# Performance work log

Hardware: AMD Instinct MI355X
Metric: run time of the kernel (lower is better)

The kernel has to match this reference:

```python
import jax, jax.numpy as jnp
import numpy as np

N_NODES = 50000
N_EDGES = 600000
N_COMM = 500
COMM_EDGES = 8000
NFEAT = 128
NHID = 128
NCLASS = 10
NLAYERS = 3
NHEADS = 8
EPS = 1e-5


def setup_inputs() -> dict:
    key = jax.random.key(0)
    ks = jax.random.split(key, 32)
    s = 0.05
    def rn(i, shape, scale=s):
        return (jax.random.normal(ks[i], shape, dtype=jnp.float32) * scale)
    return {
        "node_features": jax.random.normal(ks[0], (N_NODES, NFEAT), dtype=jnp.float32),
        "node_edge_index": jax.random.randint(ks[1], (2, N_EDGES), 0, N_NODES),
        "comm_features": jax.random.normal(ks[2], (N_COMM, NHID), dtype=jnp.float32),
        "comm_edge_index": jax.random.randint(ks[3], (2, COMM_EDGES), 0, N_COMM),
        "node_to_comm_map": jax.random.randint(ks[4], (N_NODES,), 0, N_COMM),
        # node-branch GCN params (nfeat == nhid so weights stack)
        "node_W": rn(5, (NLAYERS, NHID, NHID)),
        "node_b": rn(6, (NLAYERS, NHID)),
        "node_bn_g": 1.0 + rn(7, (NLAYERS, NHID)),
        "node_bn_b": rn(8, (NLAYERS, NHID)),
        # community-branch GCN params
        "comm_W": rn(9, (NLAYERS, NHID, NHID)),
        "comm_b": rn(10, (NLAYERS, NHID)),
        "comm_bn_g": 1.0 + rn(11, (NLAYERS, NHID)),
        "comm_bn_b": rn(12, (NLAYERS, NHID)),
        # MultiheadAttention params (torch layout: y = x @ W.T + b)
        "attn_in_w": rn(13, (3 * NHID, NHID)),
        "attn_in_b": rn(14, (3 * NHID,)),
        "attn_out_w": rn(15, (NHID, NHID)),
        "attn_out_b": rn(16, (NHID,)),
        # gate LayerNorm
        "ln_g": 1.0 + rn(17, (NHID,)),
        "ln_b": rn(18, (NHID,)),
        # classifier: Linear(128,64) -> BN -> ReLU -> Linear(64,10)
        "cls_W1": rn(19, (NHID, NHID // 2)),
        "cls_b1": rn(20, (NHID // 2,)),
        "cls_bn_g": 1.0 + rn(21, (NHID // 2,)),
        "cls_bn_b": rn(22, (NHID // 2,)),
        "cls_W2": rn(23, (NHID // 2, NCLASS)),
        "cls_b2": rn(24, (NCLASS,)),
    }


def _gcn_norm(edge_index, n):
    # PyG gcn_norm: add self-loops, symmetric D^-1/2 (A+I) D^-1/2
    loop = jnp.arange(n)
    src = jnp.concatenate([edge_index[0], loop])
    dst = jnp.concatenate([edge_index[1], loop])
    deg = jax.ops.segment_sum(jnp.ones(src.shape[0], jnp.float32), dst, num_segments=n)
    dinv = jnp.where(deg > 0, deg ** -0.5, 0.0)
    return src, dst, dinv[src] * dinv[dst]


def _gcn_stack(x, edge_index, Ws, bs, gs, betas):
    n = x.shape[0]
    src, dst, norm = _gcn_norm(edge_index, n)
    h = x
    for i in range(Ws.shape[0]):
        h_prev = h
        m = h @ Ws[i]  # linear commutes with normalized aggregation
        agg = jax.ops.segment_sum(m[src] * norm[:, None], dst, num_segments=n) + bs[i]
        mu = agg.mean(0)
        var = agg.var(0)  # biased, as torch BN training
        hb = (agg - mu) / jnp.sqrt(var + EPS) * gs[i] + betas[i]
        h = jax.nn.relu(hb)
        if i > 0:
            h = h + h_prev
    return h


def _mha(x, wi, bi, wo, bo):
    # x: [N, S=2, E]
    N, S, E = x.shape
    dh = E // NHEADS
    qkv = x @ wi.T + bi
    q, k, v = jnp.split(qkv, 3, axis=-1)
    q = q.reshape(N, S, NHEADS, dh)
    k = k.reshape(N, S, NHEADS, dh)
    v = v.reshape(N, S, NHEADS, dh)
    att = jnp.einsum('nqhd,nkhd->nhqk', q, k) / np.float32(np.sqrt(dh))
    att = jax.nn.softmax(att, axis=-1)
    o = jnp.einsum('nhqk,nkhd->nqhd', att, v).reshape(N, S, E)
    return o @ wo.T + bo


def reference(node_features, node_edge_index, comm_features, comm_edge_index,
              node_to_comm_map, node_W, node_b, node_bn_g, node_bn_b,
              comm_W, comm_b, comm_bn_g, comm_bn_b,
              attn_in_w, attn_in_b, attn_out_w, attn_out_b,
              ln_g, ln_b, cls_W1, cls_b1, cls_bn_g, cls_bn_b, cls_W2, cls_b2):
    h_node = _gcn_stack(node_features, node_edge_index, node_W, node_b, node_bn_g, node_bn_b)
    h_comm = _gcn_stack(comm_features, comm_edge_index, comm_W, comm_b, comm_bn_g, comm_bn_b)
    safe = jnp.clip(node_to_comm_map, 0, h_comm.shape[0] - 1)
    h_comm_exp = h_comm[safe]  # [N, nhid] cross-scale gather
    comb = jnp.stack([h_node, h_comm_exp], axis=1)  # [N, 2, nhid]
    attended = _mha(comb, attn_in_w, attn_in_b, attn_out_w, attn_out_b)
    x = attended.mean(axis=1) + h_node
    mu = x.mean(-1, keepdims=True)
    var = x.var(-1, keepdims=True)
    h_final = (x - mu) / jnp.sqrt(var + EPS) * ln_g + ln_b
    z = h_final @ cls_W1 + cls_b1
    zm = z.mean(0)
    zv = z.var(0)
    z = jax.nn.relu((z - zm) / jnp.sqrt(zv + EPS) * cls_bn_g + cls_bn_b)
    logits = z @ cls_W2 + cls_b2
    return jax.nn.log_softmax(logits, axis=-1)
```

## Files before the change

kernel.cpp:

```cpp
#include <hip/hip_runtime.h>
#include <hip/hip_bf16.h>
#include <cstdint>
#include <cstddef>


typedef __attribute__((ext_vector_type(8))) short bf16x8;
typedef __attribute__((ext_vector_type(4))) float f32x4;

#define EPSV 1e-5f

__device__ __forceinline__ float b2f(unsigned short u) {
    union { unsigned int i; float f; } x; x.i = ((unsigned int)u) << 16; return x.f;
}
__device__ __forceinline__ unsigned short f2b(float f) {
    union { float f; unsigned int i; } x; x.f = f;
    unsigned int i = x.i;
    return (unsigned short)((i + 0x7fffu + ((i >> 16) & 1u)) >> 16);
}

__global__ void prep_kernel(const float* __restrict__ node_W, const float* __restrict__ comm_W,
                            const float* __restrict__ cls_W1, const float* __restrict__ attn_in_w,
                            const float* __restrict__ attn_out_w, const float* __restrict__ comm_feat,
                            const float* __restrict__ node_feat,
                            unsigned short* __restrict__ WtN, unsigned short* __restrict__ WtC,
                            unsigned short* __restrict__ W1t, unsigned short* __restrict__ WinB,
                            unsigned short* __restrict__ WoutB, unsigned short* __restrict__ cfb,
                            unsigned short* __restrict__ nfb, int nC128, int nN128) {
    int idx = blockIdx.x * 256 + threadIdx.x;
    if (idx < 49152) {
        int l = idx >> 14, e = idx & 16383;
        int j = e & 7, lane = (e >> 3) & 63, kc = (e >> 9) & 3, t = e >> 11;
        int col = t * 16 + (lane & 15);
        int k = (lane >> 4) * 8 + kc * 32 + j;
        WtN[idx] = f2b(node_W[l * 16384 + k * 128 + col]); return;
    }
    idx -= 49152;
    if (idx < 49152) {
        int l = idx >> 14, e = idx & 16383;
        int j = e & 7, lane = (e >> 3) & 63, kc = (e >> 9) & 3, t = e >> 11;
        int col = t * 16 + (lane & 15);
        int k = (lane >> 4) * 8 + kc * 32 + j;
        WtC[idx] = f2b(comm_W[l * 16384 + k * 128 + col]); return;
    }
    idx -= 49152;
    if (idx < 8192) {
        int e = idx;
        int j = e & 7, lane = (e >> 3) & 63, kc = (e >> 9) & 3, t = e >> 11;
        int col = t * 16 + (lane & 15);
        int k = (lane >> 4) * 8 + kc * 32 + j;
        W1t[idx] = f2b(cls_W1[k * 64 + col]); return;
    }
    idx -= 8192;
    if (idx < 49152) {
        int e = idx;
        int j = e & 7, lane = (e >> 3) & 63, kc = (e >> 9) & 3, t = e >> 11;
        int col = t * 16 + (lane & 15);
        int k = (lane >> 4) * 8 + kc * 32 + j;
        WinB[idx] = f2b(attn_in_w[col * 128 + k]); return;
    }
    idx -= 49152;
    if (idx < 16384) {
        int e = idx;
        int j = e & 7, lane = (e >> 3) & 63, kc = (e >> 9) & 3, t = e >> 11;
        int col = t * 16 + (lane & 15);
        int k = (lane >> 4) * 8 + kc * 32 + j;
        WoutB[idx] = f2b(attn_out_w[col * 128 + k]); return;
    }
    idx -= 16384;
    if (idx < nC128) { cfb[idx] = f2b(comm_feat[idx]); return; }
    idx -= nC128;
    if (idx < nN128) { nfb[idx] = f2b(node_feat[idx]); }
}

__global__ void count_dual(const int* __restrict__ nd, int* __restrict__ cnt_n, int nE,
                           const int* __restrict__ cd, int* __restrict__ cnt_c, int cE) {
    int t = blockIdx.x * 256 + threadIdx.x;
    if (t < nE) atomicAdd(&cnt_n[nd[t]], 1);
    else if (t - nE < cE) atomicAdd(&cnt_c[cd[t - nE]], 1);
}

__global__ void dinv_dual(const int* __restrict__ cnt_n, float* __restrict__ di_n, int nN,
                          const int* __restrict__ cnt_c, float* __restrict__ di_c, int nC) {
    int t = blockIdx.x * 256 + threadIdx.x;
    if (t < nN) di_n[t] = rsqrtf((float)cnt_n[t] + 1.0f);
    else if (t - nN < nC) di_c[t - nN] = rsqrtf((float)cnt_c[t - nN] + 1.0f);
}

__global__ void scan_block_dual(const int* __restrict__ cnt_n, int* __restrict__ rs_n,
                                int* __restrict__ bsum_n, int nN, int nbN,
                                const int* __restrict__ cnt_c, int* __restrict__ rs_c,
                                int* __restrict__ bsum_c, int nC) {
    __shared__ int tmp[2048];
    const int* cnt; int* excl; int* bsum; int n, lb;
    if ((int)blockIdx.x < nbN) { cnt = cnt_n; excl = rs_n; bsum = bsum_n; n = nN; lb = blockIdx.x; }
    else { cnt = cnt_c; excl = rs_c; bsum = bsum_c; n = nC; lb = blockIdx.x - nbN; }
    int tid = threadIdx.x;
    int gid = lb * 1024 + tid;
    int v = (gid < n) ? ((cnt[gid] + 7) & ~7) : 0;
    int buf = 0;
    tmp[tid] = v;
    __syncthreads();
    for (int d = 1; d < 1024; d <<= 1) {
        int t = tmp[buf * 1024 + tid];
        int add = (tid >= d) ? tmp[buf * 1024 + tid - d] : 0;
        tmp[(1 - buf) * 1024 + tid] = t + add;
        buf = 1 - buf;
        __syncthreads();
    }
    int inc = tmp[buf * 1024 + tid];
    if (gid < n) excl[gid] = inc - v;
    if (tid == 1023) bsum[lb] = inc;
}

__global__ void scan_sums_dual(int* __restrict__ bsum_n, int nbN,
                               int* __restrict__ bsum_c, int nbC) {
    if (threadIdx.x == 0) {
        int acc = 0;
        for (int i = 0; i < nbN; ++i) { int t = bsum_n[i]; bsum_n[i] = acc; acc += t; }
    } else if (threadIdx.x == 1) {
        int acc = 0;
        for (int i = 0; i < nbC; ++i) { int t = bsum_c[i]; bsum_c[i] = acc; acc += t; }
    }
}

__global__ void scan_add_dual(int* __restrict__ rs_n, const int* __restrict__ bsum_n, int nN,
                              int* __restrict__ rs_c, const int* __restrict__ bsum_c, int nC) {
    int gid = blockIdx.x * 256 + threadIdx.x;
    if (gid < nN) rs_n[gid] += bsum_n[gid >> 10];
    else {
        int g = gid - nN;
        if (g < nC) rs_c[g] += bsum_c[g >> 10];
    }
}

__global__ void fill_dual(const int* __restrict__ ns, const int* __restrict__ ndst,
                          const float* __restrict__ di_n, const int* __restrict__ rs_n,
                          int* __restrict__ cur_n, int* __restrict__ csrc_n,
                          float* __restrict__ cw_n, int nE,
                          const int* __restrict__ cs, const int* __restrict__ cdst,
                          const float* __restrict__ di_c, const int* __restrict__ rs_c,
                          int* __restrict__ cur_c, int* __restrict__ csrc_c,
                          float* __restrict__ cw_c, int cE) {
    int e = blockIdx.x * 256 + threadIdx.x;
    if (e < nE) {
        int s = ns[e], d = ndst[e];
        int pos = atomicAdd(&cur_n[d], 1);
        int slot = rs_n[d] + pos;
        csrc_n[slot] = s;
        cw_n[slot] = di_n[s] * di_n[d];
    } else if (e - nE < cE) {
        int ee = e - nE;
        int s = cs[ee], d = cdst[ee];
        int pos = atomicAdd(&cur_c[d], 1);
        int slot = rs_c[d] + pos;
        csrc_c[slot] = s;
        cw_c[slot] = di_c[s] * di_c[d];
    }
}

__device__ __forceinline__ void gemm_wave_128(const unsigned short* __restrict__ A,
                                              const unsigned short* __restrict__ Bt,
                                              unsigned short* __restrict__ D,
                                              int M, int m0, int lane) {
    int r = lane & 15, q = lane >> 4;
    int arow = m0 + r; if (arow >= M) arow = M - 1;
    const unsigned short* ap = A + (size_t)arow * 128 + q * 8;
    bf16x8 afrag[4];
#pragma unroll
    for (int kc = 0; kc < 4; ++kc)
        afrag[kc] = *(const bf16x8*)(const void*)(ap + kc * 32);
#pragma unroll
    for (int tt = 0; tt < 8; ++tt) {
        f32x4 acc = {0.f, 0.f, 0.f, 0.f};
#pragma unroll
        for (int kc = 0; kc < 4; ++kc) {
            bf16x8 bfrag = *(const bf16x8*)(const void*)(Bt + (((size_t)tt * 4 + kc) << 9) + lane * 8);
            acc = __builtin_amdgcn_mfma_f32_16x16x32_bf16(afrag[kc], bfrag, acc, 0, 0, 0);
        }
        int n0 = tt * 16;
#pragma unroll
        for (int t = 0; t < 4; ++t) {
            int row = m0 + q * 4 + t;
            if (row < M) D[(size_t)row * 128 + n0 + r] = f2b(acc[t]);
        }
    }
}

__global__ __launch_bounds__(256) void gemm_dual(
    const unsigned short* __restrict__ A0, const unsigned short* __restrict__ Bt0,
    unsigned short* __restrict__ D0, int M0, int blocksA,
    const unsigned short* __restrict__ A1, const unsigned short* __restrict__ Bt1,
    unsigned short* __restrict__ D1, int M1) {
    int blk = blockIdx.x;
    const unsigned short *A, *Bt; unsigned short* D; int M, lb;
    if (blk < blocksA) { A = A0; Bt = Bt0; D = D0; M = M0; lb = blk; }
    else { A = A1; Bt = Bt1; D = D1; M = M1; lb = blk - blocksA; }
    int m0 = (lb * 4 + (int)(threadIdx.x >> 6)) * 16;
    if (m0 >= M) return;
    gemm_wave_128(A, Bt, D, M, m0, threadIdx.x & 63);
}

__global__ void gemm_kernel(const unsigned short* __restrict__ A,
                            const unsigned short* __restrict__ Bt,
                            const float* __restrict__ bias,
                            float* __restrict__ D, int M, int Ncol) {
    int wave = (blockIdx.x * blockDim.x + threadIdx.x) >> 6;
    int lane = threadIdx.x & 63;
    int m0 = wave * 16;
    if (m0 >= M) return;
    int r = lane & 15, q = lane >> 4;
    int arow = m0 + r; if (arow >= M) arow = M - 1;
    const unsigned short* ap = A + (size_t)arow * 128 + q * 8;
    bf16x8 afrag[4];
#pragma unroll
    for (int kc = 0; kc < 4; ++kc)
        afrag[kc] = *(const bf16x8*)(const void*)(ap + kc * 32);
    int ntiles = Ncol >> 4;
    for (int tt = 0; tt < ntiles; ++tt) {
        f32x4 acc = {0.f, 0.f, 0.f, 0.f};
#pragma unroll
        for (int kc = 0; kc < 4; ++kc) {
            bf16x8 bfrag = *(const bf16x8*)(const void*)(Bt + (((size_t)tt * 4 + kc) << 9) + lane * 8);
            acc = __builtin_amdgcn_mfma_f32_16x16x32_bf16(afrag[kc], bfrag, acc, 0, 0, 0);
        }
        int n0 = tt * 16;
        float bv = bias[n0 + r];
#pragma unroll
        for (int t = 0; t < 4; ++t) {
            int row = m0 + q * 4 + t;
            if (row < M) D[(size_t)row * Ncol + n0 + r] = acc[t] + bv;
        }
    }
}

__global__ __launch_bounds__(256) void gather_dual(
    const unsigned short* __restrict__ m0, const int* __restrict__ rs0,
    const int* __restrict__ cnt0,
    const int* __restrict__ cs0, const float* __restrict__ cw0,
    const float* __restrict__ di0, const float* __restrict__ b0,
    float* __restrict__ agg0, int n0, int blocksA,
    const unsigned short* __restrict__ m1, const int* __restrict__ rs1,
    const int* __restrict__ cnt1,
    const int* __restrict__ cs1, const float* __restrict__ cw1,
    const float* __restrict__ di1, const float* __restrict__ b1,
    float* __restrict__ agg1, int n1) {
    int blk = blockIdx.x;
    const unsigned short* m; const int *rs, *cnt, *cs; const float *cw, *di, *bias;
    float *agg; int n, lb;
    if (blk < blocksA) { m = m0; rs = rs0; cnt = cnt0; cs = cs0; cw = cw0; di = di0; bias = b0; agg = agg0; n = n0; lb = blk; }
    else { m = m1; rs = rs1; cnt = cnt1; cs = cs1; cw = cw1; di = di1; bias = b1; agg = agg1; n = n1; lb = blk - blocksA; }
    int wib = threadIdx.x >> 6, lane = threadIdx.x & 63;
    int node = lb * 4 + wib;
    if (node >= n) return;
    int start = rs[node];
    int end = start + ((cnt[node] + 7) & ~7);
    float a0 = 0.f, a1 = 0.f;
    for (int i = start; i < end; i += 8) {
        int   s[8]; float w[8]; unsigned int v[8];
#pragma unroll
        for (int j = 0; j < 8; ++j) { s[j] = cs[i + j]; w[j] = cw[i + j]; }
#pragma unroll
        for (int j = 0; j < 8; ++j)
            v[j] = *(const unsigned int*)(m + (size_t)s[j] * 128 + 2 * lane);
#pragma unroll
        for (int j = 0; j < 8; ++j) {
            a0 += b2f((unsigned short)(v[j] & 0xffff)) * w[j];
            a1 += b2f((unsigned short)(v[j] >> 16)) * w[j];
        }
    }
    float d = di[node]; float wself = d * d;
    unsigned int v = *(const unsigned int*)(m + (size_t)node * 128 + 2 * lane);
    a0 += b2f((unsigned short)(v & 0xffff)) * wself + bias[2 * lane];
    a1 += b2f((unsigned short)(v >> 16)) * wself + bias[2 * lane + 1];
    float2 o; o.x = a0; o.y = a1;
    ((float2*)(agg + (size_t)node * 128))[lane] = o;
}

__global__ __launch_bounds__(256) void stats_dual(
    const float* __restrict__ agg0, float* __restrict__ sums0, int n0, int blocksA,
    const float* __restrict__ agg1, float* __restrict__ sums1, int n1) {
    __shared__ float rsum[256], rsq[256];
    int blk = blockIdx.x;
    const float* agg; float* sums; int n, lb, nb;
    if (blk < blocksA) { agg = agg0; sums = sums0; n = n0; lb = blk; nb = blocksA; }
    else { agg = agg1; sums = sums1; n = n1; lb = blk - blocksA; nb = gridDim.x - blocksA; }
    int rpb = (n + nb - 1) / nb;
    int t = threadIdx.x;
    int f = t & 127, half = t >> 7;
    int r0 = lb * rpb, r1 = r0 + rpb; if (r1 > n) r1 = n;
    float s = 0.f, s2 = 0.f;
    for (int r = r0 + half; r < r1; r += 2) {
        float v = agg[(size_t)r * 128 + f];
        s += v; s2 += v * v;
    }
    rsum[t] = s; rsq[t] = s2;
    __syncthreads();
    if (t < 128) atomicAdd(&sums[t], rsum[t] + rsum[t + 128]);
    else atomicAdd(&sums[128 + f], rsq[f] + rsq[t]);
}

__global__ __launch_bounds__(256) void apply_dual(
    const float* __restrict__ agg0, const float* __restrict__ sums0,
    const float* __restrict__ g0, const float* __restrict__ be0,
    unsigned short* __restrict__ hb0, int n0, int blocksA, int useRes,
    const float* __restrict__ agg1, const float* __restrict__ sums1,
    const float* __restrict__ g1, const float* __restrict__ be1,
    unsigned short* __restrict__ hb1, int n1) {
    __shared__ float sc[128], sh[128];
    int blk = blockIdx.x;
    const float *agg, *sums, *g, *be; unsigned short* hb; int n, lb;
    if (blk < blocksA) { agg = agg0; sums = sums0; g = g0; be = be0; hb = hb0; n = n0; lb = blk; }
    else { agg = agg1; sums = sums1; g = g1; be = be1; hb = hb1; n = n1; lb = blk - blocksA; }
    int t = threadIdx.x;
    if (t < 128) {
        float inv = 1.f / (float)n;
        float mean = sums[t] * inv;
        float var = sums[128 + t] * inv - mean * mean;
        float rstd = rsqrtf(var + EPSV);
        float s = g[t] * rstd;
        sc[t] = s;
        sh[t] = be[t] - mean * s;
    }
    __syncthreads();
    int base = lb * 1024 + t * 4;
    if (base < n * 128) {
        float4 a = *(const float4*)(agg + base);
        ushort4 h = *(const ushort4*)(hb + base);
        int f = base & 127;
        float v0 = fmaxf(a.x * sc[f] + sh[f], 0.f);
        float v1 = fmaxf(a.y * sc[f + 1] + sh[f + 1], 0.f);
        float v2 = fmaxf(a.z * sc[f + 2] + sh[f + 2], 0.f);
        float v3 = fmaxf(a.w * sc[f + 3] + sh[f + 3], 0.f);
        if (useRes) { v0 += b2f(h.x); v1 += b2f(h.y); v2 += b2f(h.z); v3 += b2f(h.w); }
        ushort4 o; o.x = f2b(v0); o.y = f2b(v1); o.z = f2b(v2); o.w = f2b(v3);
        *(ushort4*)(hb + base) = o;
    }
}

__global__ __launch_bounds__(256) void mha_fused_kernel(
    const unsigned short* __restrict__ hbn, const unsigned short* __restrict__ hbc,
    const int* __restrict__ map,
    const unsigned short* __restrict__ WinB, const float* __restrict__ bin,
    const unsigned short* __restrict__ WoutB, const float* __restrict__ bout,
    const float* __restrict__ lng, const float* __restrict__ lnb,
    unsigned short* __restrict__ hfin, int nN, int nC) {
    __shared__ unsigned short obf_s[16 * 144];
    __shared__ float att_s[8 * 132];

    int b = blockIdx.x;
    int hg = threadIdx.x >> 6;
    int lane = threadIdx.x & 63;
    int r = lane & 15, q = lane >> 4;

    int anode = b * 8 + (r >> 1);
    if (anode >= nN) anode = nN - 1;
    const unsigned short* arow;
    if (r & 1) {
        int c = map[anode]; c = c < 0 ? 0 : (c >= nC ? nC - 1 : c);
        arow = hbc + (size_t)c * 128;
    } else {
        arow = hbn + (size_t)anode * 128;
    }
    bf16x8 afrag[4];
#pragma unroll
    for (int kc = 0; kc < 4; ++kc)
        afrag[kc] = *(const bf16x8*)(const void*)(arow + q * 8 + kc * 32);

    f32x4 qa[2], ka[2], va[2];
#pragma unroll
    for (int p = 0; p < 3; ++p) {
#pragma unroll
        for (int c = 0; c < 2; ++c) {
            int tt = p * 8 + hg * 2 + c;
            f32x4 acc = {0.f, 0.f, 0.f, 0.f};
#pragma unroll
            for (int kc = 0; kc < 4; ++kc) {
                bf16x8 bfrag = *(const bf16x8*)(const void*)(WinB + (((size_t)tt * 4 + kc) << 9) + lane * 8);
                acc = __builtin_amdgcn_mfma_f32_16x16x32_bf16(afrag[kc], bfrag, acc, 0, 0, 0);
            }
            float bv = bin[tt * 16 + r];
#pragma unroll
            for (int t = 0; t < 4; ++t) acc[t] += bv;
            if (p == 0) qa[c] = acc; else if (p == 1) ka[c] = acc; else va[c] = acc;
        }
    }

#pragma unroll
    for (int c = 0; c < 2; ++c) {
        float s00 = qa[c][0] * ka[c][0], s01 = qa[c][0] * ka[c][1];
        float s10 = qa[c][1] * ka[c][0], s11 = qa[c][1] * ka[c][1];
        float u00 = qa[c][2] * ka[c][2], u01 = qa[c][2] * ka[c][3];
        float u10 = qa[c][3] * ka[c][2], u11 = qa[c][3] * ka[c][3];
#pragma unroll
        for (int mku = 1; mku <= 8; mku <<= 1) {
            s00 += __shfl_xor(s00, mku); s01 += __shfl_xor(s01, mku);
            s10 += __shfl_xor(s10, mku); s11 += __shfl_xor(s11, mku);
            u00 += __shfl_xor(u00, mku); u01 += __shfl_xor(u01, mku);
            u10 += __shfl_xor(u10, mku); u11 += __shfl_xor(u11, mku);
        }
        s00 *= 0.25f; s01 *= 0.25f; s10 *= 0.25f; s11 *= 0.25f;
        u00 *= 0.25f; u01 *= 0.25f; u10 *= 0.25f; u11 *= 0.25f;
        float m0 = fmaxf(s00, s01), m1 = fmaxf(s10, s11);
        float m2 = fmaxf(u00, u01), m3 = fmaxf(u10, u11);
        float e00 = __expf(s00 - m0), e01 = __expf(s01 - m0);
        float e10 = __expf(s10 - m1), e11 = __expf(s11 - m1);
        float f00 = __expf(u00 - m2), f01 = __expf(u01 - m2);
        float f10 = __expf(u10 - m3), f11 = __expf(u11 - m3);
        float i0 = 1.f / (e00 + e01), i1 = 1.f / (e10 + e11);
        float i2 = 1.f / (f00 + f01), i3 = 1.f / (f10 + f11);
        float o0 = (e00 * va[c][0] + e01 * va[c][1]) * i0;
        float o1 = (e10 * va[c][0] + e11 * va[c][1]) * i1;
        float o2 = (f00 * va[c][2] + f01 * va[c][3]) * i2;
        float o3 = (f10 * va[c][2] + f11 * va[c][3]) * i3;
        int ocol = (hg * 2 + c) * 16 + r;
        obf_s[(q * 4 + 0) * 144 + ocol] = f2b(o0);
        obf_s[(q * 4 + 1) * 144 + ocol] = f2b(o1);
        obf_s[(q * 4 + 2) * 144 + ocol] = f2b(o2);
        obf_s[(q * 4 + 3) * 144 + ocol] = f2b(o3);
    }
    __syncthreads();

    bf16x8 ofrag[4];
#pragma unroll
    for (int kc = 0; kc < 4; ++kc)
        ofrag[kc] = *(const bf16x8*)(const void*)(obf_s + r * 144 + q * 8 + kc * 32);
#pragma unroll
    for (int c = 0; c < 2; ++c) {
        int tt = hg * 2 + c;
        f32x4 acc = {0.f, 0.f, 0.f, 0.f};
#pragma unroll
        for (int kc = 0; kc < 4; ++kc) {
            bf16x8 bfrag = *(const bf16x8*)(const void*)(WoutB + (((size_t)tt * 4 + kc) << 9) + lane * 8);
            acc = __builtin_amdgcn_mfma_f32_16x16x32_bf16(ofrag[kc], bfrag, acc, 0, 0, 0);
        }
        int n0 = tt * 16;
        float bv = bout[n0 + r];
        att_s[(q * 2 + 0) * 132 + n0 + r] = 0.5f * (acc[0] + acc[1]) + bv;
        att_s[(q * 2 + 1) * 132 + n0 + r] = 0.5f * (acc[2] + acc[3]) + bv;
    }
    __syncthreads();

    {
        int nl = threadIdx.x >> 5;
        int j2 = threadIdx.x & 31;
        int gnode = b * 8 + nl; if (gnode >= nN) gnode = nN - 1;
        const unsigned short* hrow = hbn + (size_t)gnode * 128 + j2 * 4;
        float x[4]; float s = 0.f, s2 = 0.f;
#pragma unroll
        for (int i = 0; i < 4; ++i) {
            x[i] = att_s[nl * 132 + j2 * 4 + i] + b2f(hrow[i]);
            s += x[i]; s2 += x[i] * x[i];
        }
        s += __shfl_xor(s, 1);  s2 += __shfl_xor(s2, 1);
        s += __shfl_xor(s, 2);  s2 += __shfl_xor(s2, 2);
        s += __shfl_xor(s, 4);  s2 += __shfl_xor(s2, 4);
        s += __shfl_xor(s, 8);  s2 += __shfl_xor(s2, 8);
        s += __shfl_xor(s, 16); s2 += __shfl_xor(s2, 16);
        float mu = s * (1.f / 128.f);
        float var = s2 * (1.f / 128.f) - mu * mu;
        float rstd = rsqrtf(var + EPSV);
        ushort4 o;
        o.x = f2b((x[0] - mu) * rstd * lng[j2 * 4]     + lnb[j2 * 4]);
        o.y = f2b((x[1] - mu) * rstd * lng[j2 * 4 + 1] + lnb[j2 * 4 + 1]);
        o.z = f2b((x[2] - mu) * rstd * lng[j2 * 4 + 2] + lnb[j2 * 4 + 2]);
        o.w = f2b((x[3] - mu) * rstd * lng[j2 * 4 + 3] + lnb[j2 * 4 + 3]);
        *(ushort4*)(hfin + (size_t)gnode * 128 + j2 * 4) = o;
    }
}

__global__ __launch_bounds__(256) void stats64_kernel(const float* __restrict__ z,
                                                      float* __restrict__ sums, int N) {
    __shared__ float ls[4][64], lsq[4][64];
    int f = threadIdx.x & 63, rg = threadIdx.x >> 6;
    int r0 = blockIdx.x * 64 + rg * 16;
    int r1 = r0 + 16; if (r1 > N) r1 = N;
    float s = 0.f, s2 = 0.f;
    for (int r = r0; r < r1; ++r) {
        float v = z[(size_t)r * 64 + f];
        s += v; s2 += v * v;
    }
    ls[rg][f] = s; lsq[rg][f] = s2;
    __syncthreads();
    int t = threadIdx.x;
    if (t < 64) atomicAdd(&sums[t], ls[0][t] + ls[1][t] + ls[2][t] + ls[3][t]);
    else if (t < 128) { int c = t - 64; atomicAdd(&sums[64 + c], lsq[0][c] + lsq[1][c] + lsq[2][c] + lsq[3][c]); }
}

__global__ __launch_bounds__(256) void final_kernel(const float* __restrict__ z,
                                                    const float* __restrict__ sums,
                                                    const float* __restrict__ g,
                                                    const float* __restrict__ be,
                                                    const float* __restrict__ W2,
                                                    const float* __restrict__ b2v,
                                                    float* __restrict__ out, int nN) {
    int node = blockIdx.x * 4 + (threadIdx.x >> 6);
    int lane = threadIdx.x & 63;
    float inv = 1.f / (float)nN;
    float mean = sums[lane] * inv;
    float var = sums[64 + lane] * inv - mean * mean;
    float sc = g[lane] * rsqrtf(var + EPSV);
    float sh = be[lane] - mean * sc;
    float v = 0.f;
    if (node < nN) v = fmaxf(z[(size_t)node * 64 + lane] * sc + sh, 0.f);
    float p[10];
    const float* wrow = W2 + lane * 10;
#pragma unroll
    for (int c = 0; c < 10; ++c) p[c] = v * wrow[c];
#pragma unroll
    for (int off = 32; off >= 1; off >>= 1) {
#pragma unroll
        for (int c = 0; c < 10; ++c) p[c] += __shfl_xor(p[c], off);
    }
    if (node >= nN) return;
    float l[10], mx = -1e30f;
#pragma unroll
    for (int c = 0; c < 10; ++c) { l[c] = p[c] + b2v[c]; mx = fmaxf(mx, l[c]); }
    float se = 0.f;
#pragma unroll
    for (int c = 0; c < 10; ++c) se += expf(l[c] - mx);
    float lse = mx + logf(se);
    if (lane < 10) out[(size_t)node * 10 + lane] = l[lane] - lse;
}

static inline int cdiv(long a, long b) { return (int)((a + b - 1) / b); }

extern "C" void kernel_launch(void* const* d_in, const int* in_sizes, int n_in,
                              void* d_out, int out_size, void* d_ws, size_t ws_size,
                              hipStream_t stream) {
    const float* node_feat = (const float*)d_in[0];
    const int*   nedge     = (const int*)d_in[1];
    const float* comm_feat = (const float*)d_in[2];
    const int*   cedge     = (const int*)d_in[3];
    const int*   n2c       = (const int*)d_in[4];
    const float* node_W    = (const float*)d_in[5];
    const float* node_b    = (const float*)d_in[6];
    const float* node_g    = (const float*)d_in[7];
    const float* node_beta = (const float*)d_in[8];
    const float* comm_W    = (const float*)d_in[9];
    const float* comm_b    = (const float*)d_in[10];
    const float* comm_g    = (const float*)d_in[11];
    const float* comm_beta = (const float*)d_in[12];
    const float* attn_in_w = (const float*)d_in[13];
    const float* attn_in_b = (const float*)d_in[14];
    const float* attn_out_w= (const float*)d_in[15];
    const float* attn_out_b= (const float*)d_in[16];
    const float* ln_g      = (const float*)d_in[17];
    const float* ln_b      = (const float*)d_in[18];
    const float* cls_W1    = (const float*)d_in[19];
    const float* cls_b1    = (const float*)d_in[20];
    const float* cls_bn_g  = (const float*)d_in[21];
    const float* cls_bn_b  = (const float*)d_in[22];
    const float* cls_W2    = (const float*)d_in[23];
    const float* cls_b2    = (const float*)d_in[24];

    const int nN = in_sizes[0] / 128;
    const int nE = in_sizes[1] / 2;
    const int nC = in_sizes[2] / 128;
    const int cE = in_sizes[3] / 2;
    const int padE_n = nE + 8 * nN;
    const int padE_c = cE + 8 * nC;

    char* ws = (char*)d_ws;
    size_t off = 0;
    auto alloc = [&](size_t bytes) -> char* {
        char* p = ws + off;
        off = (off + bytes + 255) & ~(size_t)255;
        return p;
    };
    size_t zero_begin = off;
    int*   cnt_n  = (int*)alloc((size_t)nN * 4);
    int*   cur_n  = (int*)alloc((size_t)nN * 4);
    int*   cnt_c  = (int*)alloc((size_t)nC * 4);
    int*   cur_c  = (int*)alloc((size_t)nC * 4);
    float* gsums  = (float*)alloc((size_t)6 * 256 * 4);
    float* csums  = (float*)alloc(128 * 4);
    int*   csrc_n = (int*)alloc((size_t)padE_n * 4);
    float* cw_n   = (float*)alloc((size_t)padE_n * 4);
    int*   csrc_c = (int*)alloc((size_t)padE_c * 4);
    float* cw_c   = (float*)alloc((size_t)padE_c * 4);
    size_t zero_bytes = off - zero_begin;
    int*   rs_n   = (int*)alloc((size_t)(nN + 1) * 4);
    int*   bsum_n = (int*)alloc(256 * 4);
    float* dinv_n = (float*)alloc((size_t)nN * 4);
    int*   rs_c   = (int*)alloc((size_t)(nC + 1) * 4);
    int*   bsum_c = (int*)alloc(256 * 4);
    float* dinv_c = (float*)alloc((size_t)nC * 4);
    unsigned short* hb_n  = (unsigned short*)alloc((size_t)nN * 256);
    unsigned short* hb_c  = (unsigned short*)alloc((size_t)nC * 256);
    unsigned short* cfb   = (unsigned short*)alloc((size_t)nC * 256);
    unsigned short* m_cb  = (unsigned short*)alloc((size_t)nC * 256);
    float*          agg_c = (float*)alloc((size_t)nC * 512);
    unsigned short* WtN  = (unsigned short*)alloc((size_t)3 * 16384 * 2);
    unsigned short* WtC  = (unsigned short*)alloc((size_t)3 * 16384 * 2);
    unsigned short* W1t  = (unsigned short*)alloc((size_t)64 * 128 * 2);
    unsigned short* WinB = (unsigned short*)alloc((size_t)384 * 128 * 2);
    unsigned short* WoutB= (unsigned short*)alloc((size_t)128 * 128 * 2);
    unsigned short* m_nb = (unsigned short*)alloc((size_t)nN * 256);
    float*          agg_n= (float*)alloc((size_t)nN * 512);
    unsigned short* nfb  = (unsigned short*)agg_n;
    unsigned short* hfin = m_nb;
    float*          z    = agg_n;

    hipMemsetAsync(ws + zero_begin, 0, zero_bytes, stream);

    long prepN = 49152L * 3 + 8192 + 16384 + (long)nC * 128 + (long)nN * 128;
    prep_kernel<<<cdiv(prepN, 256), 256, 0, stream>>>(
        node_W, comm_W, cls_W1, attn_in_w, attn_out_w, comm_feat, node_feat,
        WtN, WtC, W1t, WinB, WoutB, cfb, nfb, nC * 128, nN * 128);

    count_dual<<<cdiv((long)nE + cE, 256), 256, 0, stream>>>(nedge + nE, cnt_n, nE, cedge + cE, cnt_c, cE);
    dinv_dual<<<cdiv((long)nN + nC, 256), 256, 0, stream>>>(cnt_n, dinv_n, nN, cnt_c, dinv_c, nC);
    int nbN = cdiv(nN, 1024), nbC = cdiv(nC, 1024);
    scan_block_dual<<<nbN + nbC, 1024, 0, stream>>>(cnt_n, rs_n, bsum_n, nN, nbN, cnt_c, rs_c, bsum_c, nC);
    scan_sums_dual<<<1, 64, 0, stream>>>(bsum_n, nbN, bsum_c, nbC);
    scan_add_dual<<<cdiv((long)nN + nC, 256), 256, 0, stream>>>(rs_n, bsum_n, nN, rs_c, bsum_c, nC);
    fill_dual<<<cdiv((long)nE + cE, 256), 256, 0, stream>>>(
        nedge, nedge + nE, dinv_n, rs_n, cur_n, csrc_n, cw_n, nE,
        cedge, cedge + cE, dinv_c, rs_c, cur_c, csrc_c, cw_c, cE);

    int gemmA = cdiv(nN, 64), gemmB = cdiv(nC, 64);
    int gatA = cdiv(nN, 4), gatB = cdiv(nC, 4);
    int appA = cdiv((long)nN * 128, 1024), appB = cdiv((long)nC * 128, 1024);
    for (int i = 0; i < 3; ++i) {
        const unsigned short* A0 = i == 0 ? nfb : hb_n;
        const unsigned short* A1 = i == 0 ? cfb : hb_c;
        float* s0 = gsums + (size_t)(i * 2 + 0) * 256;
        float* s1 = gsums + (size_t)(i * 2 + 1) * 256;
        gemm_dual<<<gemmA + gemmB, 256, 0, stream>>>(
            A0, WtN + i * 16384, m_nb, nN, gemmA,
            A1, WtC + i * 16384, m_cb, nC);
        gather_dual<<<gatA + gatB, 256, 0, stream>>>(
            m_nb, rs_n, cnt_n, csrc_n, cw_n, dinv_n, node_b + i * 128, agg_n, nN, gatA,
            m_cb, rs_c, cnt_c, csrc_c, cw_c, dinv_c, comm_b + i * 128, agg_c, nC);
        stats_dual<<<256 + 4, 256, 0, stream>>>(agg_n, s0, nN, 256, agg_c, s1, nC);
        apply_dual<<<appA + appB, 256, 0, stream>>>(
            agg_n, s0, node_g + i * 128, node_beta + i * 128, hb_n, nN, appA, i > 0 ? 1 : 0,
            agg_c, s1, comm_g + i * 128, comm_beta + i * 128, hb_c, nC);
    }

    mha_fused_kernel<<<cdiv(nN, 8), 256, 0, stream>>>(
        hb_n, hb_c, n2c, WinB, attn_in_b, WoutB, attn_out_b, ln_g, ln_b, hfin, nN, nC);

    int waves1 = (nN + 15) / 16;
    gemm_kernel<<<cdiv((long)waves1 * 64, 256), 256, 0, stream>>>(
        hfin, W1t, cls_b1, z, nN, 64);
    stats64_kernel<<<cdiv(nN, 64), 256, 0, stream>>>(z, csums, nN);
    final_kernel<<<cdiv(nN, 4), 256, 0, stream>>>(z, csums, cls_bn_g, cls_bn_b,
                                                  cls_W2, cls_b2, (float*)d_out, nN);
}
```

Before: 549.1 us.

## Precompute community QKV once and push output-mean before out-projection

```diff
diff --git a/kernel.cpp b/kernel.cpp
--- a/kernel.cpp
+++ b/kernel.cpp
@@ -338,40 +338,42 @@
 }
 
 __global__ __launch_bounds__(256) void mha_fused_kernel(
-    const unsigned short* __restrict__ hbn, const unsigned short* __restrict__ hbc,
-    const int* __restrict__ map,
+    const unsigned short* __restrict__ hbn, const int* __restrict__ map,
+    const float* __restrict__ cqkv,
     const unsigned short* __restrict__ WinB, const float* __restrict__ bin,
     const unsigned short* __restrict__ WoutB, const float* __restrict__ bout,
     const float* __restrict__ lng, const float* __restrict__ lnb,
     unsigned short* __restrict__ hfin, int nN, int nC) {
     __shared__ unsigned short obf_s[16 * 144];
-    __shared__ float att_s[8 * 132];
+    __shared__ float att_s[16 * 132];
 
     int b = blockIdx.x;
     int hg = threadIdx.x >> 6;
     int lane = threadIdx.x & 63;
     int r = lane & 15, q = lane >> 4;
 
-    int anode = b * 8 + (r >> 1);
-    if (anode >= nN) anode = nN - 1;
-    const unsigned short* arow;
-    if (r & 1) {
-        int c = map[anode]; c = c < 0 ? 0 : (c >= nC ? nC - 1 : c);
-        arow = hbc + (size_t)c * 128;
-    } else {
-        arow = hbn + (size_t)anode * 128;
-    }
+    int arow = b * 16 + r; if (arow >= nN) arow = nN - 1;
+    const unsigned short* ap = hbn + (size_t)arow * 128 + q * 8;
     bf16x8 afrag[4];
 #pragma unroll
     for (int kc = 0; kc < 4; ++kc)
-        afrag[kc] = *(const bf16x8*)(const void*)(arow + q * 8 + kc * 32);
-
-    f32x4 qa[2], ka[2], va[2];
-#pragma unroll
-    for (int p = 0; p < 3; ++p) {
-#pragma unroll
-        for (int c = 0; c < 2; ++c) {
-            int tt = p * 8 + hg * 2 + c;
+        afrag[kc] = *(const bf16x8*)(const void*)(ap + kc * 32);
+
+    const float* cp[4];
+#pragma unroll
+    for (int t = 0; t < 4; ++t) {
+        int nt = b * 16 + q * 4 + t; if (nt >= nN) nt = nN - 1;
+        int c = map[nt]; c = c < 0 ? 0 : (c >= nC ? nC - 1 : c);
+        cp[t] = cqkv + (size_t)c * 384;
+    }
+
+#pragma unroll
+    for (int c = 0; c < 2; ++c) {
+        int h = hg * 2 + c;
+        f32x4 qa, ka, va;
+#pragma unroll
+        for (int p = 0; p < 3; ++p) {
+            int tt = p * 8 + h;
             f32x4 acc = {0.f, 0.f, 0.f, 0.f};
 #pragma unroll
             for (int kc = 0; kc < 4; ++kc) {
@@ -381,42 +383,34 @@
             float bv = bin[tt * 16 + r];
 #pragma unroll
             for (int t = 0; t < 4; ++t) acc[t] += bv;
-            if (p == 0) qa[c] = acc; else if (p == 1) ka[c] = acc; else va[c] = acc;
-        }
-    }
-
-#pragma unroll
-    for (int c = 0; c < 2; ++c) {
-        float s00 = qa[c][0] * ka[c][0], s01 = qa[c][0] * ka[c][1];
-        float s10 = qa[c][1] * ka[c][0], s11 = qa[c][1] * ka[c][1];
-        float u00 = qa[c][2] * ka[c][2], u01 = qa[c][2] * ka[c][3];
-        float u10 = qa[c][3] * ka[c][2], u11 = qa[c][3] * ka[c][3];
-#pragma unroll
-        for (int mku = 1; mku <= 8; mku <<= 1) {
-            s00 += __shfl_xor(s00, mku); s01 += __shfl_xor(s01, mku);
-            s10 += __shfl_xor(s10, mku); s11 += __shfl_xor(s11, mku);
-            u00 += __shfl_xor(u00, mku); u01 += __shfl_xor(u01, mku);
-            u10 += __shfl_xor(u10, mku); u11 += __shfl_xor(u11, mku);
-        }
-        s00 *= 0.25f; s01 *= 0.25f; s10 *= 0.25f; s11 *= 0.25f;
-        u00 *= 0.25f; u01 *= 0.25f; u10 *= 0.25f; u11 *= 0.25f;
-        float m0 = fmaxf(s00, s01), m1 = fmaxf(s10, s11);
-        float m2 = fmaxf(u00, u01), m3 = fmaxf(u10, u11);
-        float e00 = __expf(s00 - m0), e01 = __expf(s01 - m0);
-        float e10 = __expf(s10 - m1), e11 = __expf(s11 - m1);
-        float f00 = __expf(u00 - m2), f01 = __expf(u01 - m2);
-        float f10 = __expf(u10 - m3), f11 = __expf(u11 - m3);
-        float i0 = 1.f / (e00 + e01), i1 = 1.f / (e10 + e11);
-        float i2 = 1.f / (f00 + f01), i3 = 1.f / (f10 + f11);
-        float o0 = (e00 * va[c][0] + e01 * va[c][1]) * i0;
-        float o1 = (e10 * va[c][0] + e11 * va[c][1]) * i1;
-        float o2 = (f00 * va[c][2] + f01 * va[c][3]) * i2;
-        float o3 = (f10 * va[c][2] + f11 * va[c][3]) * i3;
-        int ocol = (hg * 2 + c) * 16 + r;
-        obf_s[(q * 4 + 0) * 144 + ocol] = f2b(o0);
-        obf_s[(q * 4 + 1) * 144 + ocol] = f2b(o1);
-        obf_s[(q * 4 + 2) * 144 + ocol] = f2b(o2);
-        obf_s[(q * 4 + 3) * 144 + ocol] = f2b(o3);
+            if (p == 0) qa = acc; else if (p == 1) ka = acc; else va = acc;
+        }
+        float qc[4], kc_[4], vc[4];
+#pragma unroll
+        for (int t = 0; t < 4; ++t) {
+            const float* cpt = cp[t] + h * 16 + r;
+            qc[t] = cpt[0]; kc_[t] = cpt[128]; vc[t] = cpt[256];
+        }
+#pragma unroll
+        for (int t = 0; t < 4; ++t) {
+            float s00 = qa[t] * ka[t];
+            float s01 = qa[t] * kc_[t];
+            float s10 = qc[t] * ka[t];
+            float s11 = qc[t] * kc_[t];
+#pragma unroll
+            for (int mku = 1; mku <= 8; mku <<= 1) {
+                s00 += __shfl_xor(s00, mku); s01 += __shfl_xor(s01, mku);
+                s10 += __shfl_xor(s10, mku); s11 += __shfl_xor(s11, mku);
+            }
+            s00 *= 0.25f; s01 *= 0.25f; s10 *= 0.25f; s11 *= 0.25f;
+            float m0 = fmaxf(s00, s01), m1 = fmaxf(s10, s11);
+            float e00 = __expf(s00 - m0), e01 = __expf(s01 - m0);
+            float e10 = __expf(s10 - m1), e11 = __expf(s11 - m1);
+            float i0 = 1.f / (e00 + e01), i1 = 1.f / (e10 + e11);
+            float o0 = (e00 * va[t] + e01 * vc[t]) * i0;
+            float o1 = (e10 * va[t] + e11 * vc[t]) * i1;
+            obf_s[(q * 4 + t) * 144 + h * 16 + r] = f2b(0.5f * (o0 + o1));
+        }
     }
     __syncthreads();
 
@@ -435,36 +429,51 @@
         }
         int n0 = tt * 16;
         float bv = bout[n0 + r];
-        att_s[(q * 2 + 0) * 132 + n0 + r] = 0.5f * (acc[0] + acc[1]) + bv;
-        att_s[(q * 2 + 1) * 132 + n0 + r] = 0.5f * (acc[2] + acc[3]) + bv;
+#pragma unroll
+        for (int t = 0; t < 4; ++t)
+            att_s[(q * 4 + t) * 132 + n0 + r] = acc[t] + bv;
     }
     __syncthreads();
 
     {
-        int nl = threadIdx.x >> 5;
-        int j2 = threadIdx.x & 31;
-        int gnode = b * 8 + nl; if (gnode >= nN) gnode = nN - 1;
-        const unsigned short* hrow = hbn + (size_t)gnode * 128 + j2 * 4;
-        float x[4]; float s = 0.f, s2 = 0.f;
-#pragma unroll
-        for (int i = 0; i < 4; ++i) {
-            x[i] = att_s[nl * 132 + j2 * 4 + i] + b2f(hrow[i]);
-            s += x[i]; s2 += x[i] * x[i];
-        }
+        int nl = threadIdx.x >> 4;
+        int j = threadIdx.x & 15;
+        int gnode = b * 16 + nl;
+        bool ok = gnode < nN; if (!ok) gnode = nN - 1;
+        const unsigned short* hrow = hbn + (size_t)gnode * 128 + j * 8;
+        ushort4 ha = *(const ushort4*)(hrow);
+        ushort4 hbv = *(const ushort4*)(hrow + 4);
+        float x[8]; float s = 0.f, s2 = 0.f;
+        x[0] = att_s[nl * 132 + j * 8 + 0] + b2f(ha.x);
+        x[1] = att_s[nl * 132 + j * 8 + 1] + b2f(ha.y);
+        x[2] = att_s[nl * 132 + j * 8 + 2] + b2f(ha.z);
+        x[3] = att_s[nl * 132 + j * 8 + 3] + b2f(ha.w);
+        x[4] = att_s[nl * 132 + j * 8 + 4] + b2f(hbv.x);
+        x[5] = att_s[nl * 132 + j * 8 + 5] + b2f(hbv.y);
+        x[6] = att_s[nl * 132 + j * 8 + 6] + b2f(hbv.z);
+        x[7] = att_s[nl * 132 + j * 8 + 7] + b2f(hbv.w);
+#pragma unroll
+        for (int i = 0; i < 8; ++i) { s += x[i]; s2 += x[i] * x[i]; }
         s += __shfl_xor(s, 1);  s2 += __shfl_xor(s2, 1);
         s += __shfl_xor(s, 2);  s2 += __shfl_xor(s2, 2);
         s += __shfl_xor(s, 4);  s2 += __shfl_xor(s2, 4);
         s += __shfl_xor(s, 8);  s2 += __shfl_xor(s2, 8);
-        s += __shfl_xor(s, 16); s2 += __shfl_xor(s2, 16);
         float mu = s * (1.f / 128.f);
         float var = s2 * (1.f / 128.f) - mu * mu;
         float rstd = rsqrtf(var + EPSV);
-        ushort4 o;
-        o.x = f2b((x[0] - mu) * rstd * lng[j2 * 4]     + lnb[j2 * 4]);
-        o.y = f2b((x[1] - mu) * rstd * lng[j2 * 4 + 1] + lnb[j2 * 4 + 1]);
-        o.z = f2b((x[2] - mu) * rstd * lng[j2 * 4 + 2] + lnb[j2 * 4 + 2]);
-        o.w = f2b((x[3] - mu) * rstd * lng[j2 * 4 + 3] + lnb[j2 * 4 + 3]);
-        *(ushort4*)(hfin + (size_t)gnode * 128 + j2 * 4) = o;
+        if (ok) {
+            ushort4 o1, o2;
+            o1.x = f2b((x[0] - mu) * rstd * lng[j * 8 + 0] + lnb[j * 8 + 0]);
+            o1.y = f2b((x[1] - mu) * rstd * lng[j * 8 + 1] + lnb[j * 8 + 1]);
+            o1.z = f2b((x[2] - mu) * rstd * lng[j * 8 + 2] + lnb[j * 8 + 2]);
+            o1.w = f2b((x[3] - mu) * rstd * lng[j * 8 + 3] + lnb[j * 8 + 3]);
+            o2.x = f2b((x[4] - mu) * rstd * lng[j * 8 + 4] + lnb[j * 8 + 4]);
+            o2.y = f2b((x[5] - mu) * rstd * lng[j * 8 + 5] + lnb[j * 8 + 5]);
+            o2.z = f2b((x[6] - mu) * rstd * lng[j * 8 + 6] + lnb[j * 8 + 6]);
+            o2.w = f2b((x[7] - mu) * rstd * lng[j * 8 + 7] + lnb[j * 8 + 7]);
+            *(ushort4*)(hfin + (size_t)gnode * 128 + j * 8) = o1;
+            *(ushort4*)(hfin + (size_t)gnode * 128 + j * 8 + 4) = o2;
+        }
     }
 }
 
@@ -590,6 +599,7 @@
     unsigned short* cfb   = (unsigned short*)alloc((size_t)nC * 256);
     unsigned short* m_cb  = (unsigned short*)alloc((size_t)nC * 256);
     float*          agg_c = (float*)alloc((size_t)nC * 512);
+    float*          cqkv  = (float*)alloc((size_t)nC * 384 * 4);
     unsigned short* WtN  = (unsigned short*)alloc((size_t)3 * 16384 * 2);
     unsigned short* WtC  = (unsigned short*)alloc((size_t)3 * 16384 * 2);
     unsigned short* W1t  = (unsigned short*)alloc((size_t)64 * 128 * 2);
@@ -638,8 +648,12 @@
             agg_c, s1, comm_g + i * 128, comm_beta + i * 128, hb_c, nC);
     }
 
-    mha_fused_kernel<<<cdiv(nN, 8), 256, 0, stream>>>(
-        hb_n, hb_c, n2c, WinB, attn_in_b, WoutB, attn_out_b, ln_g, ln_b, hfin, nN, nC);
+    int cwaves = cdiv(nC, 16);
+    gemm_kernel<<<cdiv((long)cwaves * 64, 256), 256, 0, stream>>>(
+        hb_c, WinB, attn_in_b, cqkv, nC, 384);
+
+    mha_fused_kernel<<<cdiv(nN, 16), 256, 0, stream>>>(
+        hb_n, n2c, cqkv, WinB, attn_in_b, WoutB, attn_out_b, ln_g, ln_b, hfin, nN, nC);
 
     int waves1 = (nN + 15) / 16;
     gemm_kernel<<<cdiv((long)waves1 * 64, 256), 256, 0, stream>>>(
```

Measured after the change: 568.7 us. +3.6%, slower.
